# Kernel tuning notes

Measured on AMD Instinct MI355X. Metric: run time of the kernel, lower is better.

The kernel has to match this reference:

```python
import jax, jax.numpy as jnp
import numpy as np

N = 30000
SLOPE = 0.2  # PyG GATConv default negative_slope


def _gat_conv(x, src, dst, W, a_src, a_dst, b, heads, out_ch, concat):
    """PyG GATConv (add_self_loops already applied), eval mode (no dropout).
    x: [N, F_in]; src/dst: [E] int; W: [F_in, heads*out_ch];
    a_src/a_dst: [heads, out_ch]; b: [heads*out_ch] or [out_ch]."""
    n = x.shape[0]
    h = (x @ W).reshape(n, heads, out_ch)              # [N, H, C]
    al_src = jnp.sum(h * a_src, axis=-1)               # [N, H]
    al_dst = jnp.sum(h * a_dst, axis=-1)               # [N, H]
    e = jax.nn.leaky_relu(al_src[src] + al_dst[dst], SLOPE)  # [E, H]
    # segment softmax over incoming edges of each destination node
    m = jax.ops.segment_max(e, dst, num_segments=n)
    ex = jnp.exp(e - m[dst])
    denom = jax.ops.segment_sum(ex, dst, num_segments=n)
    alpha = ex / (denom[dst] + 1e-16)                  # [E, H]
    msg = h[src] * alpha[..., None]                    # [E, H, C]
    out = jax.ops.segment_sum(msg, dst, num_segments=n)  # [N, H, C]
    out = out.reshape(n, heads * out_ch) if concat else out.mean(axis=1)
    return out + b


def setup_inputs() -> dict:
    key = jax.random.key(0)
    ks = jax.random.split(key, 20)
    E = 480000
    IN, H0, H1, LAT = 256, 64, 128, 32
    HEADS = 4
    x = jax.random.normal(ks[0], (N, IN), dtype=jnp.float32)
    edge_index = jax.random.randint(ks[1], (2, E), 0, N, dtype=jnp.int32)

    def gp(k, fin, heads, outc, concat):
        k1, k2, k3, k4 = jax.random.split(k, 4)
        s = 0.1
        W = jax.random.normal(k1, (fin, heads * outc), dtype=jnp.float32) * s
        a_s = jax.random.normal(k2, (heads, outc), dtype=jnp.float32) * s
        a_d = jax.random.normal(k3, (heads, outc), dtype=jnp.float32) * s
        b = jax.random.normal(k4, (heads * outc if concat else outc,), dtype=jnp.float32) * s
        return W, a_s, a_d, b

    W1, as1, ad1, b1 = gp(ks[2], IN, HEADS, H0, True)
    W2, as2, ad2, b2 = gp(ks[3], H0 * HEADS, HEADS, H1, True)
    Wm, asm, adm, bm = gp(ks[4], H1 * HEADS, HEADS, LAT, False)
    Wl, asl, adl, bl = gp(ks[5], H1 * HEADS, HEADS, LAT, False)
    return dict(x=x, edge_index=edge_index,
                W1=W1, as1=as1, ad1=ad1, b1=b1,
                W2=W2, as2=as2, ad2=ad2, b2=b2,
                Wm=Wm, asm=asm, adm=adm, bm=bm,
                Wl=Wl, asl=asl, adl=adl, bl=bl)


def reference(x, edge_index, W1, as1, ad1, b1, W2, as2, ad2, b2,
              Wm, asm, adm, bm, Wl, asl, adl, bl):
    n = x.shape[0]
    # add self loops (PyG GATConv default)
    loop = jnp.arange(n, dtype=edge_index.dtype)
    src = jnp.concatenate([edge_index[0], loop])
    dst = jnp.concatenate([edge_index[1], loop])

    out = _gat_conv(x, src, dst, W1, as1, ad1, b1, heads=4, out_ch=64, concat=True)
    out = jax.nn.relu(out)
    out = _gat_conv(out, src, dst, W2, as2, ad2, b2, heads=4, out_ch=128, concat=True)
    out = jax.nn.relu(out)
    # F.dropout with training=False (eval) is identity
    z_mean = _gat_conv(out, src, dst, Wm, asm, adm, bm, heads=4, out_ch=32, concat=False)
    z_logstd = _gat_conv(out, src, dst, Wl, asl, adl, bl, heads=4, out_ch=32, concat=False)
    return z_mean, z_logstd
```

## Files before the change

### kernel.cpp

```cpp
#include <hip/hip_runtime.h>
#include <cstddef>

typedef __attribute__((ext_vector_type(8))) short short8;
typedef __attribute__((ext_vector_type(4))) float f32x4;
typedef __attribute__((ext_vector_type(8))) _Float16 half8;
typedef __attribute__((ext_vector_type(2))) _Float16 half2v;

union H8 { half8 v; half2v p[4]; unsigned int w[4]; };
union W1H2 { unsigned int w; half2v p; };

__device__ __forceinline__ unsigned short f2h(float f) {
    union { _Float16 h; unsigned short u; } x; x.h = (_Float16)f; return x.u;
}
__device__ __forceinline__ float h2f(unsigned short u) {
    union { unsigned short u; _Float16 h; } x; x.u = u; return (float)x.h;
}
__device__ __forceinline__ float lrelu(float v) { return v > 0.f ? v : 0.2f * v; }

__device__ __forceinline__ void gl_lds16(const void* g, void* l) {
    __builtin_amdgcn_global_load_lds(
        (const __attribute__((address_space(1))) void*)g,
        (__attribute__((address_space(3))) void*)l, 16, 0, 0);
}


__global__ void count_edges_kernel(const int* __restrict__ ei, int E, int N,
                                   int* __restrict__ cnt) {
    int e = blockIdx.x * blockDim.x + threadIdx.x;
    if (e >= E + N) return;
    int d = (e < E) ? ei[E + e] : (e - E);
    atomicAdd(&cnt[d], 1);
}


__global__ void scan_p1_kernel(const int* __restrict__ cnt, int* __restrict__ rp,
                               int* __restrict__ bsum, int n) {
    __shared__ int sh[256];
    int t = threadIdx.x, i = blockIdx.x * 256 + t;
    sh[t] = (i < n) ? cnt[i] : 0;
    __syncthreads();
    for (int off = 1; off < 256; off <<= 1) {
        int u = (t >= off) ? sh[t - off] : 0;
        __syncthreads();
        sh[t] += u;
        __syncthreads();
    }
    if (i < n) rp[i + 1] = sh[t];
    if (t == 255) bsum[blockIdx.x] = sh[255];
}

__global__ void scan_p3_kernel(int* __restrict__ rp, const int* __restrict__ bsum,
                               int* __restrict__ cnt, int n, int nb) {
    __shared__ int sh[256];
    int t = threadIdx.x;
    sh[t] = (t < nb) ? bsum[t] : 0;
    __syncthreads();
    for (int off = 1; off < 256; off <<= 1) {
        int u = (t >= off) ? sh[t - off] : 0;
        __syncthreads();
        sh[t] += u;
        __syncthreads();
    }
    int off = (blockIdx.x == 0) ? 0 : sh[blockIdx.x - 1];
    int i = blockIdx.x * 256 + t;
    if (i < n) {
        rp[i + 1] += off;
        cnt[i] = 0;
    }
    if (i == 0) rp[0] = 0;
}

__global__ void scatter_edges_kernel(const int* __restrict__ ei, int E, int N,
                                     const int* __restrict__ rp, int* __restrict__ cur,
                                     int* __restrict__ csrc) {
    int e = blockIdx.x * blockDim.x + threadIdx.x;
    if (e >= E + N) return;
    int s, d;
    if (e < E) { s = ei[e]; d = ei[E + e]; } else { s = e - E; d = s; }
    int pos = rp[d] + atomicAdd(&cur[d], 1);
    csrc[pos] = s;
}


__global__ void prep_kernel(
    const float* __restrict__ x, unsigned short* __restrict__ xb,
    int rows, int cols, int padRows,
    const float* __restrict__ W1, const float* __restrict__ W2,
    const float* __restrict__ Wm, const float* __restrict__ Wl,
    unsigned short* __restrict__ W1t, unsigned short* __restrict__ W2t,
    unsigned short* __restrict__ WmlT, int xBlocks) {
    if ((int)blockIdx.x < xBlocks) {
        int i = blockIdx.x * blockDim.x + threadIdx.x;
        int total = (padRows * cols) >> 2;
        if (i >= total) return;
        int r = (i * 4) / cols;
        ushort4 o;
        if (r < rows) {
            float4 v = *(const float4*)(x + (size_t)i * 4);
            o = make_ushort4(f2h(v.x), f2h(v.y), f2h(v.z), f2h(v.w));
        } else {
            o = make_ushort4(0, 0, 0, 0);
        }
        *(ushort4*)(xb + (size_t)i * 4) = o;
        return;
    }
    int i = (blockIdx.x - xBlocks) * blockDim.x + threadIdx.x;
    if (i < 65536) {
        int k = i >> 8, n = i & 255;
        W1t[(size_t)n * 256 + k] = f2h(W1[i]);
    } else if (i < 65536 + 131072) {
        int j = i - 65536;
        int k = j >> 9, n = j & 511;
        W2t[(size_t)n * 256 + k] = f2h(W2[j]);
    } else if (i < 65536 + 131072 + 65536) {
        int j = i - 196608;
        int k = j >> 7, n = j & 127;
        WmlT[(size_t)n * 512 + k] = f2h(Wm[j]);
    } else if (i < 65536 + 131072 + 131072) {
        int j = i - 262144;
        int k = j >> 7, n = j & 127;
        WmlT[(size_t)(128 + n) * 512 + k] = f2h(Wl[j]);
    }
}


__global__ __launch_bounds__(256) void gemm_f16_kernel(
    const unsigned short* __restrict__ A, const unsigned short* __restrict__ Bt,
    unsigned short* __restrict__ C, int M, int K, int Nc,
    float* __restrict__ al_s, float* __restrict__ al_d,
    const float* __restrict__ aslo, const float* __restrict__ adlo,
    const float* __restrict__ ashi, const float* __restrict__ adhi,
    int csplit, int Chead, int H) {
    __shared__ short As[64 * 32];
    __shared__ short Bs[128 * 32];
    __shared__ float salS[64][4];
    __shared__ float salD[64][4];
    int tid = threadIdx.x;
    int bm = blockIdx.y * 64;
    int bn = blockIdx.x * 128;
    int wave = tid >> 6, lane = tid & 63;
    int wm = (wave >> 1) * 32, wn = (wave & 1) * 64;
    int lm = lane & 15, lq = lane >> 4;

    f32x4 acc[2][4] = {};

    int c0 = tid, c1 = tid + 256;
    const unsigned short* Ap0 = A + (size_t)(bm + (c0 >> 2)) * K + (c0 & 3) * 8;
    const unsigned short* Bp0 = Bt + (size_t)(bn + (c0 >> 2)) * K + (c0 & 3) * 8;
    const unsigned short* Bp1 = Bt + (size_t)(bn + (c1 >> 2)) * K + (c1 & 3) * 8;

    for (int kk = 0; kk < K; kk += 32) {
        __syncthreads();
        gl_lds16(Ap0 + kk, &As[c0 * 8]);
        gl_lds16(Bp0 + kk, &Bs[c0 * 8]);
        gl_lds16(Bp1 + kk, &Bs[c1 * 8]);
        __syncthreads();
        half8 af[2], bf[4];
#pragma unroll
        for (int t = 0; t < 2; t++)
            af[t] = *(const half8*)&As[(wm + t * 16 + lm) * 32 + lq * 8];
#pragma unroll
        for (int t = 0; t < 4; t++)
            bf[t] = *(const half8*)&Bs[(wn + t * 16 + lm) * 32 + lq * 8];
#pragma unroll
        for (int tm = 0; tm < 2; tm++)
#pragma unroll
            for (int tn = 0; tn < 4; tn++)
                acc[tm][tn] = __builtin_amdgcn_mfma_f32_16x16x32_f16(
                    af[tm], bf[tn], acc[tm][tn], 0, 0, 0);
    }

#pragma unroll
    for (int tm = 0; tm < 2; tm++) {
#pragma unroll
        for (int r = 0; r < 4; r++) {
            int row = bm + wm + tm * 16 + lq * 4 + r;
            if (row < M) {
#pragma unroll
                for (int tn = 0; tn < 4; tn++) {
                    int col = bn + wn + tn * 16 + lm;
                    C[(size_t)row * Nc + col] = f2h(acc[tm][tn][r]);
                }
            }
        }
    }

    float asv[4], adv[4];
#pragma unroll
    for (int tn = 0; tn < 4; tn++) {
        int col = bn + wn + tn * 16 + lm;
        bool hi = col >= csplit;
        int cc = hi ? col - csplit : col;
        asv[tn] = hi ? ashi[cc] : aslo[cc];
        adv[tn] = hi ? adhi[cc] : adlo[cc];
    }
    int gb = wn >> 5;
#pragma unroll
    for (int tm = 0; tm < 2; tm++) {
#pragma unroll
        for (int r = 0; r < 4; r++) {
#pragma unroll
            for (int p = 0; p < 2; p++) {
                float s1 = acc[tm][2 * p][r] * asv[2 * p]
                         + acc[tm][2 * p + 1][r] * asv[2 * p + 1];
                float s2 = acc[tm][2 * p][r] * adv[2 * p]
                         + acc[tm][2 * p + 1][r] * adv[2 * p + 1];
#pragma unroll
                for (int off = 8; off >= 1; off >>= 1) {
                    s1 += __shfl_xor(s1, off);
                    s2 += __shfl_xor(s2, off);
                }
                if (lm == 0) {
                    int rl = wm + tm * 16 + lq * 4 + r;
                    salS[rl][gb + p] = s1;
                    salD[rl][gb + p] = s2;
                }
            }
        }
    }
    __syncthreads();
    if (tid < 64) {
        int row = bm + tid;
        if (row < M) {
            int hb = bn / Chead;
            int HB = 128 / Chead;
            int GH = Chead >> 5;
            for (int i = 0; i < HB; i++) {
                float ss = 0.f, sd = 0.f;
                for (int j = 0; j < GH; j++) {
                    ss += salS[tid][i * GH + j];
                    sd += salD[tid][i * GH + j];
                }
                al_s[(size_t)row * H + hb + i] = ss;
                al_d[(size_t)row * H + hb + i] = sd;
            }
        }
    }
}


template <int H4>
__global__ __launch_bounds__(256) void alpha_kernel(
    const int* __restrict__ rp, const int* __restrict__ csrc,
    const float* __restrict__ al_s, const float* __restrict__ al_d,
    unsigned short* __restrict__ alphaT, int Ep, int N) {
    const int H = 4 * H4;
    int wv = threadIdx.x >> 6;
    int lane = threadIdx.x & 63;
    int n = blockIdx.x * 4 + wv;
    if (n >= N) return;
    int beg = rp[n], end = rp[n + 1];
    int deg = end - beg;

    float ad[H];
#pragma unroll
    for (int g = 0; g < H4; g++)
        *(float4*)&ad[g * 4] = *(const float4*)(al_d + (size_t)n * H + g * 4);

    if (deg <= 64) {
        bool act = lane < deg;
        int s = act ? csrc[beg + lane] : 0;
        float v[H], m[H], ex[H], sum[H];
#pragma unroll
        for (int g = 0; g < H4; g++) {
            float4 as = *(const float4*)(al_s + (size_t)s * H + g * 4);
            v[g * 4 + 0] = lrelu(as.x + ad[g * 4 + 0]);
            v[g * 4 + 1] = lrelu(as.y + ad[g * 4 + 1]);
            v[g * 4 + 2] = lrelu(as.z + ad[g * 4 + 2]);
            v[g * 4 + 3] = lrelu(as.w + ad[g * 4 + 3]);
        }
#pragma unroll
        for (int j = 0; j < H; j++) m[j] = act ? v[j] : -3.402823466e38f;
#pragma unroll
        for (int off = 32; off >= 1; off >>= 1)
#pragma unroll
            for (int j = 0; j < H; j++) m[j] = fmaxf(m[j], __shfl_xor(m[j], off));
#pragma unroll
        for (int j = 0; j < H; j++) {
            ex[j] = act ? __expf(v[j] - m[j]) : 0.f;
            sum[j] = ex[j];
        }
#pragma unroll
        for (int off = 32; off >= 1; off >>= 1)
#pragma unroll
            for (int j = 0; j < H; j++) sum[j] += __shfl_xor(sum[j], off);
        if (act) {
#pragma unroll
            for (int j = 0; j < H; j++)
                alphaT[(size_t)j * Ep + beg + lane] = f2h(ex[j] / (sum[j] + 1e-16f));
        }
    } else {
        float m[H], sum[H];
#pragma unroll
        for (int j = 0; j < H; j++) m[j] = -3.402823466e38f;
        for (int e = beg + lane; e < end; e += 64) {
            int s = csrc[e];
#pragma unroll
            for (int g = 0; g < H4; g++) {
                float4 as = *(const float4*)(al_s + (size_t)s * H + g * 4);
                m[g * 4 + 0] = fmaxf(m[g * 4 + 0], lrelu(as.x + ad[g * 4 + 0]));
                m[g * 4 + 1] = fmaxf(m[g * 4 + 1], lrelu(as.y + ad[g * 4 + 1]));
                m[g * 4 + 2] = fmaxf(m[g * 4 + 2], lrelu(as.z + ad[g * 4 + 2]));
                m[g * 4 + 3] = fmaxf(m[g * 4 + 3], lrelu(as.w + ad[g * 4 + 3]));
            }
        }
#pragma unroll
        for (int off = 32; off >= 1; off >>= 1)
#pragma unroll
            for (int j = 0; j < H; j++) m[j] = fmaxf(m[j], __shfl_xor(m[j], off));
#pragma unroll
        for (int j = 0; j < H; j++) sum[j] = 0.f;
        for (int e = beg + lane; e < end; e += 64) {
            int s = csrc[e];
#pragma unroll
            for (int g = 0; g < H4; g++) {
                float4 as = *(const float4*)(al_s + (size_t)s * H + g * 4);
                sum[g * 4 + 0] += __expf(lrelu(as.x + ad[g * 4 + 0]) - m[g * 4 + 0]);
                sum[g * 4 + 1] += __expf(lrelu(as.y + ad[g * 4 + 1]) - m[g * 4 + 1]);
                sum[g * 4 + 2] += __expf(lrelu(as.z + ad[g * 4 + 2]) - m[g * 4 + 2]);
                sum[g * 4 + 3] += __expf(lrelu(as.w + ad[g * 4 + 3]) - m[g * 4 + 3]);
            }
        }
#pragma unroll
        for (int off = 32; off >= 1; off >>= 1)
#pragma unroll
            for (int j = 0; j < H; j++) sum[j] += __shfl_xor(sum[j], off);
        float r[H];
#pragma unroll
        for (int j = 0; j < H; j++) r[j] = 1.0f / (sum[j] + 1e-16f);
        for (int e = beg + lane; e < end; e += 64) {
            int s = csrc[e];
#pragma unroll
            for (int g = 0; g < H4; g++) {
                float4 as = *(const float4*)(al_s + (size_t)s * H + g * 4);
                alphaT[(size_t)(g * 4 + 0) * Ep + e] =
                    f2h(__expf(lrelu(as.x + ad[g * 4 + 0]) - m[g * 4 + 0]) * r[g * 4 + 0]);
                alphaT[(size_t)(g * 4 + 1) * Ep + e] =
                    f2h(__expf(lrelu(as.y + ad[g * 4 + 1]) - m[g * 4 + 1]) * r[g * 4 + 1]);
                alphaT[(size_t)(g * 4 + 2) * Ep + e] =
                    f2h(__expf(lrelu(as.z + ad[g * 4 + 2]) - m[g * 4 + 2]) * r[g * 4 + 2]);
                alphaT[(size_t)(g * 4 + 3) * Ep + e] =
                    f2h(__expf(lrelu(as.w + ad[g * 4 + 3]) - m[g * 4 + 3]) * r[g * 4 + 3]);
            }
        }
    }
}


template <int NS, int HC, int C>
__global__ __launch_bounds__(256) void agg_stage_kernel(
    const int* __restrict__ rp, const int* __restrict__ csrc,
    const unsigned short* __restrict__ alphaT, int Ep,
    const unsigned short* __restrict__ h, const float* __restrict__ bias,
    unsigned short* __restrict__ out, int N) {
    constexpr int NG = 32;
    constexpr int MAXE = 1024;
    __shared__ int lds_rp[NG + 1];
    __shared__ uint2 lds_ea[MAXE];
    int tid = threadIdx.x;
    int bs = blockIdx.x % NS;
    int g0 = (blockIdx.x / NS) * NG;
    const int hd = (bs * 64) / C;
    if (tid <= NG) {
        int nn = g0 + tid;
        lds_rp[tid] = rp[nn <= N ? nn : N];
    }
    __syncthreads();
    int e0 = lds_rp[0], span = lds_rp[NG] - e0;
    const unsigned short* at = alphaT + (size_t)hd * Ep + e0;
    bool fits = span <= MAXE;
    if (fits) {
        for (int i = tid; i < span; i += 256) {
            unsigned int off = (unsigned int)csrc[e0 + i] * (unsigned int)(HC * 2);
            unsigned int a = at[i];
            lds_ea[i] = make_uint2(off, a | (a << 16));
        }
    }
    __syncthreads();

    int grp = tid >> 3;
    int lg = tid & 7;
    int n = g0 + grp;
    if (n >= N) return;
    int ch = bs * 64 + lg * 8;
    const unsigned int lo = (unsigned int)ch * 2;
    const char* hb = (const char*)h;
    H8 A; A.v = half8{};

    if (fits) {
        int t = lds_rp[grp] - e0, end = lds_rp[grp + 1] - e0;
        for (; t + 3 < end; t += 4) {
            uint2 ea0 = lds_ea[t],     ea1 = lds_ea[t + 1];
            uint2 ea2 = lds_ea[t + 2], ea3 = lds_ea[t + 3];
            H8 h0, h1, h2, h3;
            h0.v = *(const half8*)(hb + (ea0.x + lo));
            h1.v = *(const half8*)(hb + (ea1.x + lo));
            h2.v = *(const half8*)(hb + (ea2.x + lo));
            h3.v = *(const half8*)(hb + (ea3.x + lo));
            W1H2 a0, a1, a2, a3;
            a0.w = ea0.y; a1.w = ea1.y; a2.w = ea2.y; a3.w = ea3.y;
#pragma unroll
            for (int i = 0; i < 4; i++) A.p[i] += h0.p[i] * a0.p;
#pragma unroll
            for (int i = 0; i < 4; i++) A.p[i] += h1.p[i] * a1.p;
#pragma unroll
            for (int i = 0; i < 4; i++) A.p[i] += h2.p[i] * a2.p;
#pragma unroll
            for (int i = 0; i < 4; i++) A.p[i] += h3.p[i] * a3.p;
        }
        for (; t < end; t++) {
            uint2 ea0 = lds_ea[t];
            W1H2 a0; a0.w = ea0.y;
            H8 h0; h0.v = *(const half8*)(hb + (ea0.x + lo));
#pragma unroll
            for (int i = 0; i < 4; i++) A.p[i] += h0.p[i] * a0.p;
        }
    } else {
        const unsigned short* atg = alphaT + (size_t)hd * Ep;
        for (int t = lds_rp[grp]; t < lds_rp[grp + 1]; t++) {
            unsigned int off = (unsigned int)csrc[t] * (unsigned int)(HC * 2);
            unsigned int a = atg[t];
            W1H2 a0; a0.w = a | (a << 16);
            H8 h0; h0.v = *(const half8*)(hb + (off + lo));
#pragma unroll
            for (int i = 0; i < 4; i++) A.p[i] += h0.p[i] * a0.p;
        }
    }

    short8 o;
#pragma unroll
    for (int i = 0; i < 8; i++)
        o[i] = (short)f2h(fmaxf((float)A.v[i] + bias[ch + i], 0.f));
    *(short8*)(out + (size_t)n * HC + ch) = o;
}


__global__ __launch_bounds__(256) void agg_mean_stage_kernel(
    const int* __restrict__ rp, const int* __restrict__ csrc,
    const unsigned short* __restrict__ alphaT, int Ep,
    const unsigned short* __restrict__ h,
    const float* __restrict__ bias1, const float* __restrict__ bias2,
    float* __restrict__ out1, float* __restrict__ out2, int N) {
    constexpr int NG = 16;
    constexpr int MAXE = 1024;
    __shared__ int lds_rp[NG + 1];
    __shared__ unsigned int lds_off[MAXE];
    __shared__ unsigned int lds_aw[4][MAXE];
    int tid = threadIdx.x;
    int o = blockIdx.x & 1;
    int g0 = (blockIdx.x >> 1) * NG;
    if (tid <= NG) {
        int nn = g0 + tid;
        lds_rp[tid] = rp[nn <= N ? nn : N];
    }
    __syncthreads();
    int e0 = lds_rp[0], span = lds_rp[NG] - e0;
    bool fits = span <= MAXE;
    if (fits) {
        for (int i = tid; i < span; i += 256)
            lds_off[i] = (unsigned int)csrc[e0 + i] * 512u;
#pragma unroll
        for (int hh = 0; hh < 4; hh++) {
            const unsigned short* at = alphaT + (size_t)(o * 4 + hh) * Ep + e0;
            for (int i = tid; i < span; i += 256) {
                unsigned int a = at[i];
                lds_aw[hh][i] = a | (a << 16);
            }
        }
    }
    __syncthreads();

    int grp = tid >> 4;
    int cg = tid & 15;
    int hh = cg >> 2;
    int n = g0 + grp;
    if (n >= N) return;
    int ch = o * 128 + cg * 8;
    const unsigned int lo = (unsigned int)ch * 2;
    const char* hb = (const char*)h;
    H8 A; A.v = half8{};

    if (fits) {
        int t = lds_rp[grp] - e0, end = lds_rp[grp + 1] - e0;
        for (; t + 3 < end; t += 4) {
            unsigned int o0 = lds_off[t],     o1 = lds_off[t + 1];
            unsigned int o2 = lds_off[t + 2], o3 = lds_off[t + 3];
            H8 h0, h1, h2, h3;
            h0.v = *(const half8*)(hb + (o0 + lo));
            h1.v = *(const half8*)(hb + (o1 + lo));
            h2.v = *(const half8*)(hb + (o2 + lo));
            h3.v = *(const half8*)(hb + (o3 + lo));
            W1H2 a0, a1, a2, a3;
            a0.w = lds_aw[hh][t];     a1.w = lds_aw[hh][t + 1];
            a2.w = lds_aw[hh][t + 2]; a3.w = lds_aw[hh][t + 3];
#pragma unroll
            for (int i = 0; i < 4; i++) A.p[i] += h0.p[i] * a0.p;
#pragma unroll
            for (int i = 0; i < 4; i++) A.p[i] += h1.p[i] * a1.p;
#pragma unroll
            for (int i = 0; i < 4; i++) A.p[i] += h2.p[i] * a2.p;
#pragma unroll
            for (int i = 0; i < 4; i++) A.p[i] += h3.p[i] * a3.p;
        }
        for (; t < end; t++) {
            W1H2 a0; a0.w = lds_aw[hh][t];
            H8 h0; h0.v = *(const half8*)(hb + (lds_off[t] + lo));
#pragma unroll
            for (int i = 0; i < 4; i++) A.p[i] += h0.p[i] * a0.p;
        }
    } else {
        const unsigned short* atg = alphaT + (size_t)(o * 4 + hh) * Ep;
        for (int t = lds_rp[grp]; t < lds_rp[grp + 1]; t++) {
            unsigned int off = (unsigned int)csrc[t] * 512u;
            unsigned int a = atg[t];
            W1H2 a0; a0.w = a | (a << 16);
            H8 h0; h0.v = *(const half8*)(hb + (off + lo));
#pragma unroll
            for (int i = 0; i < 4; i++) A.p[i] += h0.p[i] * a0.p;
        }
    }

    float f[8];
#pragma unroll
    for (int i = 0; i < 8; i++) f[i] = (float)A.v[i];
#pragma unroll
    for (int off = 4; off <= 8; off <<= 1)
#pragma unroll
        for (int i = 0; i < 8; i++) f[i] += __shfl_xor(f[i], off);
    if (cg < 4) {
        const float* bb = o ? bias2 : bias1;
        float* op = o ? out2 : out1;
        int wc = cg * 8;
        float4 r0, r1;
        r0.x = f[0] * 0.25f + bb[wc + 0];
        r0.y = f[1] * 0.25f + bb[wc + 1];
        r0.z = f[2] * 0.25f + bb[wc + 2];
        r0.w = f[3] * 0.25f + bb[wc + 3];
        r1.x = f[4] * 0.25f + bb[wc + 4];
        r1.y = f[5] * 0.25f + bb[wc + 5];
        r1.z = f[6] * 0.25f + bb[wc + 6];
        r1.w = f[7] * 0.25f + bb[wc + 7];
        *(float4*)(op + (size_t)n * 32 + wc) = r0;
        *(float4*)(op + (size_t)n * 32 + wc + 4) = r1;
    }
}


extern "C" void kernel_launch(void* const* d_in, const int* in_sizes, int n_in,
                              void* d_out, int out_size, void* d_ws, size_t ws_size,
                              hipStream_t stream) {
    (void)n_in; (void)out_size; (void)ws_size;
    const float* x   = (const float*)d_in[0];
    const int*   ei  = (const int*)d_in[1];
    const float* W1  = (const float*)d_in[2];
    const float* as1 = (const float*)d_in[3];
    const float* ad1 = (const float*)d_in[4];
    const float* b1  = (const float*)d_in[5];
    const float* W2  = (const float*)d_in[6];
    const float* as2 = (const float*)d_in[7];
    const float* ad2 = (const float*)d_in[8];
    const float* b2  = (const float*)d_in[9];
    const float* Wm  = (const float*)d_in[10];
    const float* a_sm = (const float*)d_in[11];
    const float* a_dm = (const float*)d_in[12];
    const float* bm  = (const float*)d_in[13];
    const float* Wl  = (const float*)d_in[14];
    const float* a_sl = (const float*)d_in[15];
    const float* a_dl = (const float*)d_in[16];
    const float* bl  = (const float*)d_in[17];
    float* outp = (float*)d_out;

    const int N  = in_sizes[0] / 256;
    const int E  = in_sizes[1] / 2;
    const int ET = E + N;
    const int gM128 = (N + 127) / 128;
    const int Mp = gM128 * 128;
    const int gM64 = (N + 63) / 64;
    const int nSB = (N + 255) / 256;

    auto align_up = [](size_t v) { return (v + 255) & ~(size_t)255; };
    char* w = (char*)d_ws;
    int* row_ptr = (int*)w;  w += align_up((size_t)(N + 1) * 4);
    int* cnt     = (int*)w;  w += align_up((size_t)N * 4);
    int* bsum    = (int*)w;  w += align_up((size_t)nSB * 4);
    int* csrc    = (int*)w;  w += align_up((size_t)ET * 4);
    float* al_s  = (float*)w; w += align_up((size_t)N * 8 * 4);
    float* al_d  = (float*)w; w += align_up((size_t)N * 8 * 4);
    unsigned short* xb   = (unsigned short*)w; w += align_up((size_t)Mp * 256 * 2);
    unsigned short* W1t  = (unsigned short*)w; w += align_up((size_t)256 * 256 * 2);
    unsigned short* W2t  = (unsigned short*)w; w += align_up((size_t)512 * 256 * 2);
    unsigned short* WmlT = (unsigned short*)w; w += align_up((size_t)256 * 512 * 2);
    unsigned short* bufH = (unsigned short*)w; w += align_up((size_t)Mp * 512 * 2);
    unsigned short* bufO = (unsigned short*)w; w += align_up((size_t)Mp * 512 * 2);
    unsigned short* alphaT = xb;

    int gzE = (ET + 255) / 256;
    hipMemsetAsync(cnt, 0, (size_t)N * 4, stream);
    count_edges_kernel<<<gzE, 256, 0, stream>>>(ei, E, N, cnt);
    scan_p1_kernel<<<nSB, 256, 0, stream>>>(cnt, row_ptr, bsum, N);
    scan_p3_kernel<<<nSB, 256, 0, stream>>>(row_ptr, bsum, cnt, N, nSB);
    scatter_edges_kernel<<<gzE, 256, 0, stream>>>(ei, E, N, row_ptr, cnt, csrc);

    int xBlocks = ((Mp * 256 / 4) + 255) / 256;
    int wBlocks = (393216 + 255) / 256;
    prep_kernel<<<xBlocks + wBlocks, 256, 0, stream>>>(
        x, xb, N, 256, Mp, W1, W2, Wm, Wl, W1t, W2t, WmlT, xBlocks);

    int gF = (N + 3) / 4;
    int gB = (N + 31) / 32;
    int gB2 = (N + 15) / 16;

    gemm_f16_kernel<<<dim3(2, gM64), 256, 0, stream>>>(
        xb, W1t, bufH, N, 256, 256, al_s, al_d, as1, ad1, as1, ad1, 256, 64, 4);
    alpha_kernel<1><<<gF, 256, 0, stream>>>(row_ptr, csrc, al_s, al_d, alphaT, ET, N);
    agg_stage_kernel<4, 256, 64><<<4 * gB, 256, 0, stream>>>(
        row_ptr, csrc, alphaT, ET, bufH, b1, bufO, N);

    gemm_f16_kernel<<<dim3(4, gM64), 256, 0, stream>>>(
        bufO, W2t, bufH, N, 256, 512, al_s, al_d, as2, ad2, as2, ad2, 512, 128, 4);
    alpha_kernel<1><<<gF, 256, 0, stream>>>(row_ptr, csrc, al_s, al_d, alphaT, ET, N);
    agg_stage_kernel<8, 512, 128><<<8 * gB, 256, 0, stream>>>(
        row_ptr, csrc, alphaT, ET, bufH, b2, bufO, N);

    gemm_f16_kernel<<<dim3(2, gM64), 256, 0, stream>>>(
        bufO, WmlT, bufH, N, 512, 256, al_s, al_d, a_sm, a_dm, a_sl, a_dl, 128, 32, 8);
    alpha_kernel<2><<<gF, 256, 0, stream>>>(row_ptr, csrc, al_s, al_d, alphaT, ET, N);
    agg_mean_stage_kernel<<<2 * gB2, 256, 0, stream>>>(
        row_ptr, csrc, alphaT, ET, bufH, bm, bl, outp, outp + (size_t)N * 32, N);
}
```

Measured before the change: 403.3 us.

## Dynamically assign destination nodes to thread groups via LDS work queue

The aggregation kernels now cover twice as many destination nodes per block, and each 8- or 16-lane group pulls its next node from a shared LDS atomic counter instead of owning one fixed node. The goal is to balance uneven in-degrees within a block so groups stop idling while the longest node finishes, and to amortize the edge-staging cost over more nodes. The cost is an LDS atomic and shuffle per node, a larger LDS edge buffer for the concat kernel, and half as many blocks, which may lower occupancy.

```diff
diff --git a/kernel.cpp b/kernel.cpp
--- a/kernel.cpp
+++ b/kernel.cpp
@@ -31,7 +31,6 @@
     int d = (e < E) ? ei[E + e] : (e - E);
     atomicAdd(&cnt[d], 1);
 }
-
 
 __global__ void scan_p1_kernel(const int* __restrict__ cnt, int* __restrict__ rp,
                                int* __restrict__ bsum, int n) {
@@ -353,10 +352,11 @@
     const unsigned short* __restrict__ alphaT, int Ep,
     const unsigned short* __restrict__ h, const float* __restrict__ bias,
     unsigned short* __restrict__ out, int N) {
-    constexpr int NG = 32;
-    constexpr int MAXE = 1024;
+    constexpr int NG = 64;
+    constexpr int MAXE = 2048;
     __shared__ int lds_rp[NG + 1];
     __shared__ uint2 lds_ea[MAXE];
+    __shared__ int lds_q;
     int tid = threadIdx.x;
     int bs = blockIdx.x % NS;
     int g0 = (blockIdx.x / NS) * NG;
@@ -365,6 +365,7 @@
         int nn = g0 + tid;
         lds_rp[tid] = rp[nn <= N ? nn : N];
     }
+    if (tid == 0) lds_q = 0;
     __syncthreads();
     int e0 = lds_rp[0], span = lds_rp[NG] - e0;
     const unsigned short* at = alphaT + (size_t)hd * Ep + e0;
@@ -378,60 +379,66 @@
     }
     __syncthreads();
 
-    int grp = tid >> 3;
     int lg = tid & 7;
-    int n = g0 + grp;
-    if (n >= N) return;
     int ch = bs * 64 + lg * 8;
     const unsigned int lo = (unsigned int)ch * 2;
     const char* hb = (const char*)h;
-    H8 A; A.v = half8{};
-
-    if (fits) {
-        int t = lds_rp[grp] - e0, end = lds_rp[grp + 1] - e0;
-        for (; t + 3 < end; t += 4) {
-            uint2 ea0 = lds_ea[t],     ea1 = lds_ea[t + 1];
-            uint2 ea2 = lds_ea[t + 2], ea3 = lds_ea[t + 3];
-            H8 h0, h1, h2, h3;
-            h0.v = *(const half8*)(hb + (ea0.x + lo));
-            h1.v = *(const half8*)(hb + (ea1.x + lo));
-            h2.v = *(const half8*)(hb + (ea2.x + lo));
-            h3.v = *(const half8*)(hb + (ea3.x + lo));
-            W1H2 a0, a1, a2, a3;
-            a0.w = ea0.y; a1.w = ea1.y; a2.w = ea2.y; a3.w = ea3.y;
-#pragma unroll
-            for (int i = 0; i < 4; i++) A.p[i] += h0.p[i] * a0.p;
-#pragma unroll
-            for (int i = 0; i < 4; i++) A.p[i] += h1.p[i] * a1.p;
-#pragma unroll
-            for (int i = 0; i < 4; i++) A.p[i] += h2.p[i] * a2.p;
-#pragma unroll
-            for (int i = 0; i < 4; i++) A.p[i] += h3.p[i] * a3.p;
-        }
-        for (; t < end; t++) {
-            uint2 ea0 = lds_ea[t];
-            W1H2 a0; a0.w = ea0.y;
-            H8 h0; h0.v = *(const half8*)(hb + (ea0.x + lo));
-#pragma unroll
-            for (int i = 0; i < 4; i++) A.p[i] += h0.p[i] * a0.p;
-        }
-    } else {
-        const unsigned short* atg = alphaT + (size_t)hd * Ep;
-        for (int t = lds_rp[grp]; t < lds_rp[grp + 1]; t++) {
-            unsigned int off = (unsigned int)csrc[t] * (unsigned int)(HC * 2);
-            unsigned int a = atg[t];
-            W1H2 a0; a0.w = a | (a << 16);
-            H8 h0; h0.v = *(const half8*)(hb + (off + lo));
-#pragma unroll
-            for (int i = 0; i < 4; i++) A.p[i] += h0.p[i] * a0.p;
-        }
-    }
-
-    short8 o;
-#pragma unroll
-    for (int i = 0; i < 8; i++)
-        o[i] = (short)f2h(fmaxf((float)A.v[i] + bias[ch + i], 0.f));
-    *(short8*)(out + (size_t)n * HC + ch) = o;
+    const unsigned short* atg = alphaT + (size_t)hd * Ep;
+
+    for (;;) {
+        int ln;
+        if (lg == 0) ln = atomicAdd(&lds_q, 1);
+        ln = __shfl(ln, (threadIdx.x & 63) & 56);
+        if (ln >= NG) break;
+        int n = g0 + ln;
+        if (n >= N) break;
+        H8 A; A.v = half8{};
+
+        if (fits) {
+            int t = lds_rp[ln] - e0, end = lds_rp[ln + 1] - e0;
+            for (; t + 3 < end; t += 4) {
+                uint2 ea0 = lds_ea[t],     ea1 = lds_ea[t + 1];
+                uint2 ea2 = lds_ea[t + 2], ea3 = lds_ea[t + 3];
+                H8 h0, h1, h2, h3;
+                h0.v = *(const half8*)(hb + (ea0.x + lo));
+                h1.v = *(const half8*)(hb + (ea1.x + lo));
+                h2.v = *(const half8*)(hb + (ea2.x + lo));
+                h3.v = *(const half8*)(hb + (ea3.x + lo));
+                W1H2 a0, a1, a2, a3;
+                a0.w = ea0.y; a1.w = ea1.y; a2.w = ea2.y; a3.w = ea3.y;
+#pragma unroll
+                for (int i = 0; i < 4; i++) A.p[i] += h0.p[i] * a0.p;
+#pragma unroll
+                for (int i = 0; i < 4; i++) A.p[i] += h1.p[i] * a1.p;
+#pragma unroll
+                for (int i = 0; i < 4; i++) A.p[i] += h2.p[i] * a2.p;
+#pragma unroll
+                for (int i = 0; i < 4; i++) A.p[i] += h3.p[i] * a3.p;
+            }
+            for (; t < end; t++) {
+                uint2 ea0 = lds_ea[t];
+                W1H2 a0; a0.w = ea0.y;
+                H8 h0; h0.v = *(const half8*)(hb + (ea0.x + lo));
+#pragma unroll
+                for (int i = 0; i < 4; i++) A.p[i] += h0.p[i] * a0.p;
+            }
+        } else {
+            for (int t = lds_rp[ln]; t < lds_rp[ln + 1]; t++) {
+                unsigned int off = (unsigned int)csrc[t] * (unsigned int)(HC * 2);
+                unsigned int a = atg[t];
+                W1H2 a0; a0.w = a | (a << 16);
+                H8 h0; h0.v = *(const half8*)(hb + (off + lo));
+#pragma unroll
+                for (int i = 0; i < 4; i++) A.p[i] += h0.p[i] * a0.p;
+            }
+        }
+
+        short8 o;
+#pragma unroll
+        for (int i = 0; i < 8; i++)
+            o[i] = (short)f2h(fmaxf((float)A.v[i] + bias[ch + i], 0.f));
+        *(short8*)(out + (size_t)n * HC + ch) = o;
+    }
 }
 
 
@@ -441,11 +448,12 @@
     const unsigned short* __restrict__ h,
     const float* __restrict__ bias1, const float* __restrict__ bias2,
     float* __restrict__ out1, float* __restrict__ out2, int N) {
-    constexpr int NG = 16;
+    constexpr int NG = 32;
     constexpr int MAXE = 1024;
     __shared__ int lds_rp[NG + 1];
     __shared__ unsigned int lds_off[MAXE];
     __shared__ unsigned int lds_aw[4][MAXE];
+    __shared__ int lds_q;
     int tid = threadIdx.x;
     int o = blockIdx.x & 1;
     int g0 = (blockIdx.x >> 1) * NG;
@@ -453,6 +461,7 @@
         int nn = g0 + tid;
         lds_rp[tid] = rp[nn <= N ? nn : N];
     }
+    if (tid == 0) lds_q = 0;
     __syncthreads();
     int e0 = lds_rp[0], span = lds_rp[NG] - e0;
     bool fits = span <= MAXE;
@@ -470,78 +479,84 @@
     }
     __syncthreads();
 
-    int grp = tid >> 4;
     int cg = tid & 15;
     int hh = cg >> 2;
-    int n = g0 + grp;
-    if (n >= N) return;
     int ch = o * 128 + cg * 8;
     const unsigned int lo = (unsigned int)ch * 2;
     const char* hb = (const char*)h;
-    H8 A; A.v = half8{};
-
-    if (fits) {
-        int t = lds_rp[grp] - e0, end = lds_rp[grp + 1] - e0;
-        for (; t + 3 < end; t += 4) {
-            unsigned int o0 = lds_off[t],     o1 = lds_off[t + 1];
-            unsigned int o2 = lds_off[t + 2], o3 = lds_off[t + 3];
-            H8 h0, h1, h2, h3;
-            h0.v = *(const half8*)(hb + (o0 + lo));
-            h1.v = *(const half8*)(hb + (o1 + lo));
-            h2.v = *(const half8*)(hb + (o2 + lo));
-            h3.v = *(const half8*)(hb + (o3 + lo));
-            W1H2 a0, a1, a2, a3;
-            a0.w = lds_aw[hh][t];     a1.w = lds_aw[hh][t + 1];
-            a2.w = lds_aw[hh][t + 2]; a3.w = lds_aw[hh][t + 3];
-#pragma unroll
-            for (int i = 0; i < 4; i++) A.p[i] += h0.p[i] * a0.p;
-#pragma unroll
-            for (int i = 0; i < 4; i++) A.p[i] += h1.p[i] * a1.p;
-#pragma unroll
-            for (int i = 0; i < 4; i++) A.p[i] += h2.p[i] * a2.p;
-#pragma unroll
-            for (int i = 0; i < 4; i++) A.p[i] += h3.p[i] * a3.p;
-        }
-        for (; t < end; t++) {
-            W1H2 a0; a0.w = lds_aw[hh][t];
-            H8 h0; h0.v = *(const half8*)(hb + (lds_off[t] + lo));
-#pragma unroll
-            for (int i = 0; i < 4; i++) A.p[i] += h0.p[i] * a0.p;
-        }
-    } else {
-        const unsigned short* atg = alphaT + (size_t)(o * 4 + hh) * Ep;
-        for (int t = lds_rp[grp]; t < lds_rp[grp + 1]; t++) {
-            unsigned int off = (unsigned int)csrc[t] * 512u;
-            unsigned int a = atg[t];
-            W1H2 a0; a0.w = a | (a << 16);
-            H8 h0; h0.v = *(const half8*)(hb + (off + lo));
-#pragma unroll
-            for (int i = 0; i < 4; i++) A.p[i] += h0.p[i] * a0.p;
-        }
-    }
-
-    float f[8];
-#pragma unroll
-    for (int i = 0; i < 8; i++) f[i] = (float)A.v[i];
-#pragma unroll
-    for (int off = 4; off <= 8; off <<= 1)
-#pragma unroll
-        for (int i = 0; i < 8; i++) f[i] += __shfl_xor(f[i], off);
-    if (cg < 4) {
-        const float* bb = o ? bias2 : bias1;
-        float* op = o ? out2 : out1;
-        int wc = cg * 8;
-        float4 r0, r1;
-        r0.x = f[0] * 0.25f + bb[wc + 0];
-        r0.y = f[1] * 0.25f + bb[wc + 1];
-        r0.z = f[2] * 0.25f + bb[wc + 2];
-        r0.w = f[3] * 0.25f + bb[wc + 3];
-        r1.x = f[4] * 0.25f + bb[wc + 4];
-        r1.y = f[5] * 0.25f + bb[wc + 5];
-        r1.z = f[6] * 0.25f + bb[wc + 6];
-        r1.w = f[7] * 0.25f + bb[wc + 7];
-        *(float4*)(op + (size_t)n * 32 + wc) = r0;
-        *(float4*)(op + (size_t)n * 32 + wc + 4) = r1;
+    const unsigned short* atg = alphaT + (size_t)(o * 4 + hh) * Ep;
+
+    for (;;) {
+        int ln;
+        if (cg == 0) ln = atomicAdd(&lds_q, 1);
+        ln = __shfl(ln, (threadIdx.x & 63) & 48);
+        if (ln >= NG) break;
+        int n = g0 + ln;
+        if (n >= N) break;
+        H8 A; A.v = half8{};
+
+        if (fits) {
+            int t = lds_rp[ln] - e0, end = lds_rp[ln + 1] - e0;
+            for (; t + 3 < end; t += 4) {
+                unsigned int o0 = lds_off[t],     o1 = lds_off[t + 1];
+                unsigned int o2 = lds_off[t + 2], o3 = lds_off[t + 3];
+                H8 h0, h1, h2, h3;
+                h0.v = *(const half8*)(hb + (o0 + lo));
+                h1.v = *(const half8*)(hb + (o1 + lo));
+                h2.v = *(const half8*)(hb + (o2 + lo));
+                h3.v = *(const half8*)(hb + (o3 + lo));
+                W1H2 a0, a1, a2, a3;
+                a0.w = lds_aw[hh][t];     a1.w = lds_aw[hh][t + 1];
+                a2.w = lds_aw[hh][t + 2]; a3.w = lds_aw[hh][t + 3];
+#pragma unroll
+                for (int i = 0; i < 4; i++) A.p[i] += h0.p[i] * a0.p;
+#pragma unroll
+                for (int i = 0; i < 4; i++) A.p[i] += h1.p[i] * a1.p;
+#pragma unroll
+                for (int i = 0; i < 4; i++) A.p[i] += h2.p[i] * a2.p;
+#pragma unroll
+                for (int i = 0; i < 4; i++) A.p[i] += h3.p[i] * a3.p;
+            }
+            for (; t < end; t++) {
+                W1H2 a0; a0.w = lds_aw[hh][t];
+                H8 h0; h0.v = *(const half8*)(hb + (lds_off[t] + lo));
+#pragma unroll
+                for (int i = 0; i < 4; i++) A.p[i] += h0.p[i] * a0.p;
+            }
+        } else {
+            for (int t = lds_rp[ln]; t < lds_rp[ln + 1]; t++) {
+                unsigned int off = (unsigned int)csrc[t] * 512u;
+                unsigned int a = atg[t];
+                W1H2 a0; a0.w = a | (a << 16);
+                H8 h0; h0.v = *(const half8*)(hb + (off + lo));
+#pragma unroll
+                for (int i = 0; i < 4; i++) A.p[i] += h0.p[i] * a0.p;
+            }
+        }
+
+        float f[8];
+#pragma unroll
+        for (int i = 0; i < 8; i++) f[i] = (float)A.v[i];
+#pragma unroll
+        for (int off = 4; off <= 8; off <<= 1)
+#pragma unroll
+            for (int i = 0; i < 8; i++) f[i] += __shfl_xor(f[i], off);
+        if (cg < 4) {
+            const float* bb = o ? bias2 : bias1;
+            float* op = o ? out2 : out1;
+            int wc = cg * 8;
+            float4 r0, r1;
+            r0.x = f[0] * 0.25f + bb[wc + 0];
+            r0.y = f[1] * 0.25f + bb[wc + 1];
+            r0.z = f[2] * 0.25f + bb[wc + 2];
+            r0.w = f[3] * 0.25f + bb[wc + 3];
+            r1.x = f[4] * 0.25f + bb[wc + 4];
+            r1.y = f[5] * 0.25f + bb[wc + 5];
+            r1.z = f[6] * 0.25f + bb[wc + 6];
+            r1.w = f[7] * 0.25f + bb[wc + 7];
+            *(float4*)(op + (size_t)n * 32 + wc) = r0;
+            *(float4*)(op + (size_t)n * 32 + wc + 4) = r1;
+        }
     }
 }
 
@@ -607,8 +622,8 @@
         x, xb, N, 256, Mp, W1, W2, Wm, Wl, W1t, W2t, WmlT, xBlocks);
 
     int gF = (N + 3) / 4;
-    int gB = (N + 31) / 32;
-    int gB2 = (N + 15) / 16;
+    int gB = (N + 63) / 64;
+    int gB2 = (N + 31) / 32;
 
     gemm_f16_kernel<<<dim3(2, gM64), 256, 0, stream>>>(
         xb, W1t, bufH, N, 256, 256, al_s, al_d, as1, ad1, as1, ad1, 256, 64, 4);
```

Measured after the change: 407.3 us. Within noise of the previous version (+1.0%).

## Double GEMM K-tile to 64 and XOR-swizzle LDS layout to cut bank conflicts

Applied to the files above, without the earlier changes.

The f16 MFMA GEMM now stages a 64-wide K slice per iteration instead of 32, halving the number of barrier pairs per K loop. It also applies an XOR swizzle on the LDS column offset, both when loading via global_load_lds and when reading fragments, so that the 16-byte fragment reads avoid bank conflicts. LDS use per block doubles, which may lower occupancy, and K must be a multiple of 64.

```diff
diff --git a/kernel.cpp b/kernel.cpp
--- a/kernel.cpp
+++ b/kernel.cpp
@@ -31,7 +31,6 @@
     int d = (e < E) ? ei[E + e] : (e - E);
     atomicAdd(&cnt[d], 1);
 }
-
 
 __global__ void scan_p1_kernel(const int* __restrict__ cnt, int* __restrict__ rp,
                                int* __restrict__ bsum, int n) {
@@ -131,8 +130,8 @@
     const float* __restrict__ aslo, const float* __restrict__ adlo,
     const float* __restrict__ ashi, const float* __restrict__ adhi,
     int csplit, int Chead, int H) {
-    __shared__ short As[64 * 32];
-    __shared__ short Bs[128 * 32];
+    __shared__ short As[64 * 64];
+    __shared__ short Bs[128 * 64];
     __shared__ float salS[64][4];
     __shared__ float salD[64][4];
     int tid = threadIdx.x;
@@ -144,30 +143,43 @@
 
     f32x4 acc[2][4] = {};
 
-    int c0 = tid, c1 = tid + 256;
-    const unsigned short* Ap0 = A + (size_t)(bm + (c0 >> 2)) * K + (c0 & 3) * 8;
-    const unsigned short* Bp0 = Bt + (size_t)(bn + (c0 >> 2)) * K + (c0 & 3) * 8;
-    const unsigned short* Bp1 = Bt + (size_t)(bn + (c1 >> 2)) * K + (c1 & 3) * 8;
-
-    for (int kk = 0; kk < K; kk += 32) {
+    int wr = tid >> 3;
+    int wkb = (tid & 7) * 8;
+    int swz = wkb ^ ((wr & 7) * 8);
+    const unsigned short* Ar0 = A + (size_t)(bm + wr) * K + swz;
+    const unsigned short* Ar1 = A + (size_t)(bm + 32 + wr) * K + swz;
+    const unsigned short* Br0 = Bt + (size_t)(bn + wr) * K + swz;
+    const unsigned short* Br1 = Bt + (size_t)(bn + 32 + wr) * K + swz;
+    const unsigned short* Br2 = Bt + (size_t)(bn + 64 + wr) * K + swz;
+    const unsigned short* Br3 = Bt + (size_t)(bn + 96 + wr) * K + swz;
+    const int rswz = (lm & 7) * 8;
+
+    for (int kk = 0; kk < K; kk += 64) {
         __syncthreads();
-        gl_lds16(Ap0 + kk, &As[c0 * 8]);
-        gl_lds16(Bp0 + kk, &Bs[c0 * 8]);
-        gl_lds16(Bp1 + kk, &Bs[c1 * 8]);
+        gl_lds16(Ar0 + kk, &As[tid * 8]);
+        gl_lds16(Ar1 + kk, &As[2048 + tid * 8]);
+        gl_lds16(Br0 + kk, &Bs[tid * 8]);
+        gl_lds16(Br1 + kk, &Bs[2048 + tid * 8]);
+        gl_lds16(Br2 + kk, &Bs[4096 + tid * 8]);
+        gl_lds16(Br3 + kk, &Bs[6144 + tid * 8]);
         __syncthreads();
-        half8 af[2], bf[4];
-#pragma unroll
-        for (int t = 0; t < 2; t++)
-            af[t] = *(const half8*)&As[(wm + t * 16 + lm) * 32 + lq * 8];
-#pragma unroll
-        for (int t = 0; t < 4; t++)
-            bf[t] = *(const half8*)&Bs[(wn + t * 16 + lm) * 32 + lq * 8];
-#pragma unroll
-        for (int tm = 0; tm < 2; tm++)
-#pragma unroll
-            for (int tn = 0; tn < 4; tn++)
-                acc[tm][tn] = __builtin_amdgcn_mfma_f32_16x16x32_f16(
-                    af[tm], bf[tn], acc[tm][tn], 0, 0, 0);
+#pragma unroll
+        for (int ks = 0; ks < 2; ks++) {
+            int kb = (ks * 32 + lq * 8) ^ rswz;
+            half8 af[2], bf[4];
+#pragma unroll
+            for (int t = 0; t < 2; t++)
+                af[t] = *(const half8*)&As[(wm + t * 16 + lm) * 64 + kb];
+#pragma unroll
+            for (int t = 0; t < 4; t++)
+                bf[t] = *(const half8*)&Bs[(wn + t * 16 + lm) * 64 + kb];
+#pragma unroll
+            for (int tm = 0; tm < 2; tm++)
+#pragma unroll
+                for (int tn = 0; tn < 4; tn++)
+                    acc[tm][tn] = __builtin_amdgcn_mfma_f32_16x16x32_f16(
+                        af[tm], bf[tn], acc[tm][tn], 0, 0, 0);
+        }
     }
 
 #pragma unroll
```

New measurement: 397.6 us. Within noise of the previous version (-1.4%).
